# Optimization experiments

Measured on AMD Instinct MI355X. Metric: run time of the kernel, lower is better.

The kernel has to match this reference:

```python
import jax, jax.numpy as jnp
import numpy as np

N, L, S, D, H, DK = 4, 2048, 2048, 1024, 16, 64


def setup_inputs() -> dict:
    key = jax.random.key(0)
    kq, kk, kv, kwq, kwo = jax.random.split(key, 5)
    Q = jax.random.normal(kq, (N, L, D), dtype=jnp.float32)
    K = jax.random.normal(kk, (N, S, D), dtype=jnp.float32)
    V = jax.random.normal(kv, (N, S, D), dtype=jnp.float32)
    # per-head query projection weights (the source reuses Lq for K and V too)
    Wq = jax.random.normal(kwq, (H, DK, D), dtype=jnp.float32) * (D ** -0.5)
    # output projection Lo: Linear(h*dv -> Dv), weight shape (out, in)
    Wo = jax.random.normal(kwo, (D, H * DK), dtype=jnp.float32) * ((H * DK) ** -0.5)
    return {"Q": Q, "K": K, "V": V, "Wq": Wq, "Wo": Wo}


def reference(Q, K, V, Wq, Wo):
    dk = Wq.shape[1]
    # Faithful to source: ALL of q, k, v are projected with the Lq weights.
    q = jnp.einsum('nld,hkd->hnlk', Q, Wq)   # (H,N,L,dk)
    k = jnp.einsum('nsd,hkd->hnsk', K, Wq)   # (H,N,S,dk)
    v = jnp.einsum('nsd,hkd->hnsk', V, Wq)   # (H,N,S,dk)
    scale = jnp.asarray(dk, Q.dtype) ** 0.5
    scores = jnp.einsum('hnlk,hnsk->hnls', q, k) / scale  # (H,N,L,S)
    # Faithful to F.softmax(dot) with no dim on a 3D tensor: torch picks dim=0
    # (the batch axis N); here that is axis=1 of the head-stacked (H,N,L,S).
    attn = jax.nn.softmax(scores, axis=1)
    heads = jnp.einsum('hnls,hnsk->hnlk', attn, v)        # (H,N,L,dk)
    # concat heads along last dim -> (N,L,H*dk)
    heads = jnp.transpose(heads, (1, 2, 0, 3)).reshape(Q.shape[0], Q.shape[1], -1)
    return heads @ Wo.T  # (N,L,Dv)
```

## Files before the change

### kernel.cpp

```cpp
#include <hip/hip_runtime.h>
#include <hip/hip_bf16.h>

typedef __attribute__((ext_vector_type(8))) short short8;
typedef __attribute__((ext_vector_type(4))) short short4v;
typedef __attribute__((ext_vector_type(4))) float float4v;

#define DEVI static __device__ __forceinline__

#if __has_builtin(__builtin_amdgcn_exp2f)
#define EXP2(x) __builtin_amdgcn_exp2f(x)
#else
#define EXP2(x) exp2f(x)
#endif

DEVI unsigned short f2bf(float f) {
  unsigned int u = __builtin_bit_cast(unsigned int, f);
  u += 0x7fffu + ((u >> 16) & 1u);
  return (unsigned short)(u >> 16);
}

DEVI short8 pack8(float4v a, float4v b) {
  struct P4 { __hip_bfloat162 x, y, z, w; } t;
  t.x = __float22bfloat162_rn(make_float2(a[0], a[1]));
  t.y = __float22bfloat162_rn(make_float2(a[2], a[3]));
  t.z = __float22bfloat162_rn(make_float2(b[0], b[1]));
  t.w = __float22bfloat162_rn(make_float2(b[2], b[3]));
  short8 r;
  __builtin_memcpy(&r, &t, 16);
  return r;
}

DEVI short4v pack4(float a, float b, float c, float d) {
  struct P2 { __hip_bfloat162 x, y; } t;
  t.x = __float22bfloat162_rn(make_float2(a, b));
  t.y = __float22bfloat162_rn(make_float2(c, d));
  short4v r;
  __builtin_memcpy(&r, &t, 8);
  return r;
}

DEVI void gload16(const void* src, void* lds_dst) {
  __builtin_amdgcn_global_load_lds(
      (const __attribute__((address_space(1))) void*)src,
      (__attribute__((address_space(3))) void*)lds_dst, 16, 0, 0);
}

template<int AF32, int CMODE>
__global__ __launch_bounds__(256, 2)
void gemm_bt128(const void* __restrict__ Ap, const float* __restrict__ Bp,
                void* __restrict__ Cp, int M, int Nc, int Kd, float oscale)
{
  __shared__ alignas(16) short As[128 * 40];
  __shared__ alignas(16) short Bs[128 * 40];

  const int tid = threadIdx.x;
  const int lane = tid & 63;
  const int wid = tid >> 6;
  const int rl = lane & 15;
  const int g = lane >> 4;
  const int bm = blockIdx.x * 128;
  const int bn = blockIdx.y * 128;
  const int wm = (wid >> 1) * 64;
  const int wn = (wid & 1) * 64;
  const int srow = tid >> 1;
  const int k0 = (tid & 1) * 16;

  float4v acc[4][4];
#pragma unroll
  for (int i = 0; i < 4; ++i)
#pragma unroll
    for (int j = 0; j < 4; ++j) acc[i][j] = (float4v)(0.0f);

  const float* Af = (const float*)Ap;
  const unsigned short* Ab = (const unsigned short*)Ap;

  float4v afr[4], bfr[4];
  short8 ah[2], bh[2];

  const int NK = Kd >> 5;

  auto loadA = [&](int ks) {
    size_t base = (size_t)(bm + srow) * Kd + ks * 32 + k0;
    if constexpr (AF32 != 0) {
      afr[0] = *(const float4v*)(Af + base);
      afr[1] = *(const float4v*)(Af + base + 4);
      afr[2] = *(const float4v*)(Af + base + 8);
      afr[3] = *(const float4v*)(Af + base + 12);
    } else {
      ah[0] = *(const short8*)(Ab + base);
      ah[1] = *(const short8*)(Ab + base + 8);
    }
  };
  auto loadB = [&](int ks) {
    size_t base = (size_t)(bn + srow) * Kd + ks * 32 + k0;
    bfr[0] = *(const float4v*)(Bp + base);
    bfr[1] = *(const float4v*)(Bp + base + 4);
    bfr[2] = *(const float4v*)(Bp + base + 8);
    bfr[3] = *(const float4v*)(Bp + base + 12);
  };

  loadA(0);
  loadB(0);

  for (int ks = 0; ks < NK; ++ks) {
    if constexpr (AF32 != 0) {
      ah[0] = pack8(afr[0], afr[1]);
      ah[1] = pack8(afr[2], afr[3]);
    }
    bh[0] = pack8(bfr[0], bfr[1]);
    bh[1] = pack8(bfr[2], bfr[3]);
    __syncthreads();
    *(short8*)(As + srow * 40 + k0)     = ah[0];
    *(short8*)(As + srow * 40 + k0 + 8) = ah[1];
    *(short8*)(Bs + srow * 40 + k0)     = bh[0];
    *(short8*)(Bs + srow * 40 + k0 + 8) = bh[1];
    __syncthreads();
    if (ks + 1 < NK) { loadA(ks + 1); loadB(ks + 1); }

    short8 a8[4], b8[4];
#pragma unroll
    for (int mt = 0; mt < 4; ++mt)
      a8[mt] = *(const short8*)(As + (wm + mt * 16 + rl) * 40 + 8 * g);
#pragma unroll
    for (int nt = 0; nt < 4; ++nt)
      b8[nt] = *(const short8*)(Bs + (wn + nt * 16 + rl) * 40 + 8 * g);
#pragma unroll
    for (int mt = 0; mt < 4; ++mt)
#pragma unroll
      for (int nt = 0; nt < 4; ++nt)
        acc[mt][nt] = __builtin_amdgcn_mfma_f32_16x16x32_bf16(a8[mt], b8[nt], acc[mt][nt], 0, 0, 0);
  }

#pragma unroll
  for (int mt = 0; mt < 4; ++mt)
#pragma unroll
    for (int nt = 0; nt < 4; ++nt) {
      const int col = bn + wn + nt * 16 + rl;
      const int row0 = bm + wm + mt * 16 + 4 * g;
      if constexpr (CMODE == 1) {
        float* C = (float*)Cp;
#pragma unroll
        for (int r = 0; r < 4; ++r)
          C[(size_t)(row0 + r) * Nc + col] = acc[mt][nt][r];
      } else if constexpr (CMODE == 0) {
        unsigned short* C = (unsigned short*)Cp;
#pragma unroll
        for (int r = 0; r < 4; ++r)
          C[(size_t)(row0 + r) * Nc + col] = f2bf(acc[mt][nt][r] * oscale);
      } else {
        unsigned short* C = (unsigned short*)Cp;
        short4v w = pack4(acc[mt][nt][0], acc[mt][nt][1], acc[mt][nt][2], acc[mt][nt][3]);
        *(short4v*)(C + (size_t)col * M + row0) = w;
      }
    }
}

__global__ __launch_bounds__(512, 2)
void attn_bn(const unsigned short* __restrict__ qb,
             const unsigned short* __restrict__ kb,
             const unsigned short* __restrict__ vtb,
             unsigned short* __restrict__ hb)
{
  __shared__ alignas(128) char smem[131072];

  const int tid = threadIdx.x;
  const int lane = tid & 63;
  const int wid = tid >> 6;
  const int rl = lane & 15;
  const int g = lane >> 4;
  const int h = blockIdx.y;
  const int l0 = blockIdx.x * 128 + wid * 16;

  short8 qf[4][2];
#pragma unroll
  for (int n = 0; n < 4; ++n)
#pragma unroll
    for (int dh = 0; dh < 2; ++dh)
      qf[n][dh] = *(const short8*)(qb + (size_t)(n * 2048 + l0 + rl) * 1024 + h * 64 + dh * 32 + 8 * g);

  float4v ha[4][4];
#pragma unroll
  for (int n = 0; n < 4; ++n)
#pragma unroll
    for (int t = 0; t < 4; ++t) ha[n][t] = (float4v)(0.0f);

  const size_t koff0 = ((size_t)(wid * 2048) + (size_t)(lane >> 3)) * 1024
                     + (size_t)(h * 64) + (size_t)(((lane & 7) ^ (lane >> 3)) * 8);
  const size_t voff0 = ((size_t)(h * 64) + (size_t)(lane >> 2)) * 8192
                     + (size_t)((wid - 4) * 2048)
                     + (size_t)((((lane & 3) ^ ((lane >> 3) & 3)) * 8));

  auto stage = [&](int step, int b) {
    if (wid < 4) {
      char* kdst = smem + b * 32768 + wid * 4096;
      const unsigned short* ksrc = kb + koff0 + (size_t)step * 32 * 1024;
#pragma unroll
      for (int ii = 0; ii < 4; ++ii)
        gload16(ksrc + ii * 8192, kdst + ii * 1024);
    } else {
      char* vdst = smem + b * 32768 + 16384 + (wid - 4) * 4096;
      const unsigned short* vsrc = vtb + voff0 + (size_t)step * 32;
#pragma unroll
      for (int ii = 0; ii < 4; ++ii)
        gload16(vsrc + (size_t)ii * 16 * 8192, vdst + ii * 1024);
    }
  };

  stage(0, 0);
  stage(1, 1);
  stage(2, 2);
  asm volatile("s_waitcnt vmcnt(8)" ::: "memory");
  __builtin_amdgcn_s_barrier();

  const unsigned xr = ((unsigned)((rl >> 1) & 3)) << 4;
  const unsigned half = ((unsigned)(g & 1)) << 3;
  const unsigned voff_lo = (((((unsigned)g >> 1) << 4) ^ xr) + half);
  const unsigned voff_hi = ((((2u + ((unsigned)g >> 1)) << 4) ^ xr) + half);

  for (int to = 0; to < 16; ++to) {
#pragma unroll
    for (int ti = 0; ti < 4; ++ti) {
      const int t = to * 4 + ti;
      char* kbase = smem + ti * 32768;
      char* vbase = kbase + 16384;

      float4v sc[4][2];
#pragma unroll
      for (int n = 0; n < 4; ++n) {
        char* kn = kbase + n * 4096;
#pragma unroll
        for (int ss = 0; ss < 2; ++ss) {
          const int srw = ss * 16 + rl;
          const unsigned sw = ((unsigned)(srw & 7)) << 4;
          short8 kf0 = *(const short8*)(kn + srw * 128 + ((16u * (unsigned)g) ^ sw));
          short8 kf1 = *(const short8*)(kn + srw * 128 + ((64u + 16u * (unsigned)g) ^ sw));
          float4v c = (float4v)(0.0f);
          c = __builtin_amdgcn_mfma_f32_16x16x32_bf16(kf0, qf[n][0], c, 0, 0, 0);
          c = __builtin_amdgcn_mfma_f32_16x16x32_bf16(kf1, qf[n][1], c, 0, 0, 0);
          sc[n][ss] = c;
        }
      }

      short4v pf[2][4];
#pragma unroll
      for (int ss = 0; ss < 2; ++ss) {
        float ex[4][4];
#pragma unroll
        for (int n = 0; n < 4; ++n)
#pragma unroll
          for (int r = 0; r < 4; ++r)
            ex[n][r] = EXP2(fminf(sc[n][ss][r], 24.0f));
#pragma unroll
        for (int r = 0; r < 4; ++r) {
          float inv = __builtin_amdgcn_rcpf((ex[0][r] + ex[1][r]) + (ex[2][r] + ex[3][r]) + 1e-30f);
          ex[0][r] *= inv; ex[1][r] *= inv; ex[2][r] *= inv; ex[3][r] *= inv;
        }
#pragma unroll
        for (int n = 0; n < 4; ++n)
          pf[ss][n] = pack4(ex[n][0], ex[n][1], ex[n][2], ex[n][3]);
      }

#pragma unroll
      for (int n = 0; n < 4; ++n) {
        char* vn = vbase + n * 4096;
        short8 pf8 = __builtin_shufflevector(pf[0][n], pf[1][n], 0, 1, 2, 3, 4, 5, 6, 7);
#pragma unroll
        for (int t4 = 0; t4 < 4; ++t4) {
          const char* rowp = vn + (t4 * 16 + rl) * 64;
          short4v lo = *(const short4v*)(rowp + voff_lo);
          short4v hi = *(const short4v*)(rowp + voff_hi);
          short8 va8 = __builtin_shufflevector(lo, hi, 0, 1, 2, 3, 4, 5, 6, 7);
          ha[n][t4] = __builtin_amdgcn_mfma_f32_16x16x32_bf16(va8, pf8, ha[n][t4], 0, 0, 0);
        }
      }

      if (t + 3 < 64) stage(t + 3, (ti + 3) & 3);
      asm volatile("s_waitcnt vmcnt(8)" ::: "memory");
      __builtin_amdgcn_s_barrier();
    }
  }

#pragma unroll
  for (int n = 0; n < 4; ++n)
#pragma unroll
    for (int tt = 0; tt < 4; ++tt) {
      short4v w = pack4(ha[n][tt][0], ha[n][tt][1], ha[n][tt][2], ha[n][tt][3]);
      size_t off = (size_t)(n * 2048 + l0 + rl) * 1024 + h * 64 + tt * 16 + 4 * g;
      *(short4v*)(hb + off) = w;
    }
}

extern "C" void kernel_launch(void* const* d_in, const int* in_sizes, int n_in,
                              void* d_out, int out_size, void* d_ws, size_t ws_size,
                              hipStream_t stream)
{
  const float* Q  = (const float*)d_in[0];
  const float* K  = (const float*)d_in[1];
  const float* V  = (const float*)d_in[2];
  const float* Wq = (const float*)d_in[3];
  const float* Wo = (const float*)d_in[4];
  float* out = (float*)d_out;

  unsigned short* qb = (unsigned short*)d_ws;
  unsigned short* kw = qb + (size_t)8192 * 1024;
  unsigned short* vt = kw + (size_t)8192 * 1024;
  unsigned short* hw = qb;

  const float CS = 0.18033688011112042f;

  dim3 gg(64, 8), bb(256);
  gemm_bt128<1, 0><<<gg, bb, 0, stream>>>(Q, Wq, qb, 8192, 1024, 1024, CS);
  gemm_bt128<1, 0><<<gg, bb, 0, stream>>>(K, Wq, kw, 8192, 1024, 1024, 1.0f);
  gemm_bt128<1, 2><<<gg, bb, 0, stream>>>(V, Wq, vt, 8192, 1024, 1024, 1.0f);
  attn_bn<<<dim3(16, 16), dim3(512), 0, stream>>>(qb, kw, vt, hw);
  gemm_bt128<0, 1><<<gg, bb, 0, stream>>>(hw, Wo, out, 8192, 1024, 1024, 1.0f);
}
```

Baseline: 274.8 us.

## Split attention over key range with atomic fp32 accumulation and smaller LDS

Splits the attention kernel's key dimension in two across a new grid z axis, doubling block count. It halves the shared-memory ring to two stages so more blocks fit per CU, and replaces the bf16 head write with fp32 atomic adds into a zeroed output buffer. The output GEMM then reads fp32 heads and writes to workspace, followed by a device copy back to the output. This adds a memset, atomics, a larger fp32 intermediate read and an extra copy, and the prefetch depth drops from three stages to one.

Result: slower. 949.9 us (+245.7%).

```diff
diff --git a/kernel.cpp b/kernel.cpp
--- a/kernel.cpp
+++ b/kernel.cpp
@@ -155,13 +155,13 @@
     }
 }
 
-__global__ __launch_bounds__(512, 2)
+__global__ __launch_bounds__(512, 4)
 void attn_bn(const unsigned short* __restrict__ qb,
              const unsigned short* __restrict__ kb,
              const unsigned short* __restrict__ vtb,
-             unsigned short* __restrict__ hb)
+             float* __restrict__ outf)
 {
-  __shared__ alignas(128) char smem[131072];
+  __shared__ alignas(128) char smem[65536];
 
   const int tid = threadIdx.x;
   const int lane = tid & 63;
@@ -169,6 +169,7 @@
   const int rl = lane & 15;
   const int g = lane >> 4;
   const int h = blockIdx.y;
+  const int z = blockIdx.z;
   const int l0 = blockIdx.x * 128 + wid * 16;
 
   short8 qf[4][2];
@@ -184,10 +185,10 @@
 #pragma unroll
     for (int t = 0; t < 4; ++t) ha[n][t] = (float4v)(0.0f);
 
-  const size_t koff0 = ((size_t)(wid * 2048) + (size_t)(lane >> 3)) * 1024
+  const size_t koff0 = ((size_t)(wid * 2048 + z * 1024) + (size_t)(lane >> 3)) * 1024
                      + (size_t)(h * 64) + (size_t)(((lane & 7) ^ (lane >> 3)) * 8);
   const size_t voff0 = ((size_t)(h * 64) + (size_t)(lane >> 2)) * 8192
-                     + (size_t)((wid - 4) * 2048)
+                     + (size_t)((wid - 4) * 2048 + z * 1024)
                      + (size_t)((((lane & 3) ^ ((lane >> 3) & 3)) * 8));
 
   auto stage = [&](int step, int b) {
@@ -207,22 +208,19 @@
   };
 
   stage(0, 0);
-  stage(1, 1);
-  stage(2, 2);
-  asm volatile("s_waitcnt vmcnt(8)" ::: "memory");
-  __builtin_amdgcn_s_barrier();
+  __syncthreads();
 
   const unsigned xr = ((unsigned)((rl >> 1) & 3)) << 4;
   const unsigned half = ((unsigned)(g & 1)) << 3;
-  const unsigned voff_lo = (((((unsigned)g >> 1) << 4) ^ xr) + half);
-  const unsigned voff_hi = ((((2u + ((unsigned)g >> 1)) << 4) ^ xr) + half);
 
   for (int to = 0; to < 16; ++to) {
 #pragma unroll
-    for (int ti = 0; ti < 4; ++ti) {
-      const int t = to * 4 + ti;
+    for (int ti = 0; ti < 2; ++ti) {
+      const int t = to * 2 + ti;
       char* kbase = smem + ti * 32768;
       char* vbase = kbase + 16384;
+
+      if (t + 1 < 32) stage(t + 1, ti ^ 1);
 
       float4v sc[4][2];
 #pragma unroll
@@ -241,7 +239,6 @@
         }
       }
 
-      short4v pf[2][4];
 #pragma unroll
       for (int ss = 0; ss < 2; ++ss) {
         float ex[4][4];
@@ -255,28 +252,29 @@
           float inv = __builtin_amdgcn_rcpf((ex[0][r] + ex[1][r]) + (ex[2][r] + ex[3][r]) + 1e-30f);
           ex[0][r] *= inv; ex[1][r] *= inv; ex[2][r] *= inv; ex[3][r] *= inv;
         }
-#pragma unroll
-        for (int n = 0; n < 4; ++n)
-          pf[ss][n] = pack4(ex[n][0], ex[n][1], ex[n][2], ex[n][3]);
-      }
-
-#pragma unroll
-      for (int n = 0; n < 4; ++n) {
-        char* vn = vbase + n * 4096;
-        short8 pf8 = __builtin_shufflevector(pf[0][n], pf[1][n], 0, 1, 2, 3, 4, 5, 6, 7);
-#pragma unroll
-        for (int t4 = 0; t4 < 4; ++t4) {
-          const char* rowp = vn + (t4 * 16 + rl) * 64;
-          short4v lo = *(const short4v*)(rowp + voff_lo);
-          short4v hi = *(const short4v*)(rowp + voff_hi);
-          short8 va8 = __builtin_shufflevector(lo, hi, 0, 1, 2, 3, 4, 5, 6, 7);
-          ha[n][t4] = __builtin_amdgcn_mfma_f32_16x16x32_bf16(va8, pf8, ha[n][t4], 0, 0, 0);
+        short4v pf[4];
+#pragma unroll
+        for (int n = 0; n < 4; ++n) {
+          unsigned lo = (unsigned)f2bf(ex[n][0]) | ((unsigned)f2bf(ex[n][1]) << 16);
+          unsigned hi = (unsigned)f2bf(ex[n][2]) | ((unsigned)f2bf(ex[n][3]) << 16);
+          uint2 u; u.x = lo; u.y = hi;
+          pf[n] = __builtin_bit_cast(short4v, u);
+        }
+
+        const unsigned chunk0 = 2u * (unsigned)ss + ((unsigned)g >> 1);
+#pragma unroll
+        for (int n = 0; n < 4; ++n) {
+          char* vn = vbase + n * 4096;
+#pragma unroll
+          for (int t4 = 0; t4 < 4; ++t4) {
+            const char* rowp = vn + (t4 * 16 + rl) * 64;
+            short4v va = *(const short4v*)(rowp + (((chunk0 << 4) ^ xr) + half));
+            ha[n][t4] = __builtin_amdgcn_mfma_f32_16x16x16bf16_1k(va, pf[n], ha[n][t4], 0, 0, 0);
+          }
         }
       }
 
-      if (t + 3 < 64) stage(t + 3, (ti + 3) & 3);
-      asm volatile("s_waitcnt vmcnt(8)" ::: "memory");
-      __builtin_amdgcn_s_barrier();
+      __syncthreads();
     }
   }
 
@@ -284,9 +282,10 @@
   for (int n = 0; n < 4; ++n)
 #pragma unroll
     for (int tt = 0; tt < 4; ++tt) {
-      short4v w = pack4(ha[n][tt][0], ha[n][tt][1], ha[n][tt][2], ha[n][tt][3]);
       size_t off = (size_t)(n * 2048 + l0 + rl) * 1024 + h * 64 + tt * 16 + 4 * g;
-      *(short4v*)(hb + off) = w;
+#pragma unroll
+      for (int r = 0; r < 4; ++r)
+        unsafeAtomicAdd(outf + off + r, ha[n][tt][r]);
     }
 }
 
@@ -304,14 +303,17 @@
   unsigned short* qb = (unsigned short*)d_ws;
   unsigned short* kw = qb + (size_t)8192 * 1024;
   unsigned short* vt = kw + (size_t)8192 * 1024;
-  unsigned short* hw = qb;
+  float* cbuf = (float*)d_ws;
 
   const float CS = 0.18033688011112042f;
 
   dim3 gg(64, 8), bb(256);
+  hipMemsetAsync(d_out, 0, (size_t)out_size * sizeof(float), stream);
   gemm_bt128<1, 0><<<gg, bb, 0, stream>>>(Q, Wq, qb, 8192, 1024, 1024, CS);
   gemm_bt128<1, 0><<<gg, bb, 0, stream>>>(K, Wq, kw, 8192, 1024, 1024, 1.0f);
   gemm_bt128<1, 2><<<gg, bb, 0, stream>>>(V, Wq, vt, 8192, 1024, 1024, 1.0f);
-  attn_bn<<<dim3(16, 16), dim3(512), 0, stream>>>(qb, kw, vt, hw);
-  gemm_bt128<0, 1><<<gg, bb, 0, stream>>>(hw, Wo, out, 8192, 1024, 1024, 1.0f);
-}
+  attn_bn<<<dim3(16, 16, 2), dim3(512), 0, stream>>>(qb, kw, vt, (float*)d_out);
+  gemm_bt128<1, 1><<<gg, bb, 0, stream>>>(d_out, Wo, cbuf, 8192, 1024, 1024, 1.0f);
+  hipMemcpyAsync(d_out, cbuf, (size_t)out_size * sizeof(float),
+                 hipMemcpyDeviceToDevice, stream);
+}
```

## Double-buffer GEMM LDS tiles and split PV MFMA into per-half 16x16x16 ops

Applied to the files above, without the earlier changes.

The projection GEMM now keeps two LDS buffers and writes the next tile after the current MFMAs. This drops one barrier per k-step and lets the LDS stores overlap compute. In attention, the PV product is issued per score half as 16x16x16 MFMAs as soon as each half's probabilities are packed, instead of building an 8-wide operand from both halves. That shortens register live ranges and removes the shuffles, but doubles the MFMA instruction count and doubles LDS use in the GEMM, which may hurt occupancy.

Result: no change. 273.5 us (-0.5%).

```diff
diff --git a/kernel.cpp b/kernel.cpp
--- a/kernel.cpp
+++ b/kernel.cpp
@@ -50,8 +50,8 @@
 void gemm_bt128(const void* __restrict__ Ap, const float* __restrict__ Bp,
                 void* __restrict__ Cp, int M, int Nc, int Kd, float oscale)
 {
-  __shared__ alignas(16) short As[128 * 40];
-  __shared__ alignas(16) short Bs[128 * 40];
+  __shared__ alignas(16) short As[2][128 * 40];
+  __shared__ alignas(16) short Bs[2][128 * 40];
 
   const int tid = threadIdx.x;
   const int lane = tid & 63;
@@ -98,37 +98,49 @@
     bfr[2] = *(const float4v*)(Bp + base + 8);
     bfr[3] = *(const float4v*)(Bp + base + 12);
   };
-
-  loadA(0);
-  loadB(0);
-
-  for (int ks = 0; ks < NK; ++ks) {
+  auto packAB = [&]() {
     if constexpr (AF32 != 0) {
       ah[0] = pack8(afr[0], afr[1]);
       ah[1] = pack8(afr[2], afr[3]);
     }
     bh[0] = pack8(bfr[0], bfr[1]);
     bh[1] = pack8(bfr[2], bfr[3]);
-    __syncthreads();
-    *(short8*)(As + srow * 40 + k0)     = ah[0];
-    *(short8*)(As + srow * 40 + k0 + 8) = ah[1];
-    *(short8*)(Bs + srow * 40 + k0)     = bh[0];
-    *(short8*)(Bs + srow * 40 + k0 + 8) = bh[1];
-    __syncthreads();
+  };
+  auto writeLDS = [&](int b) {
+    *(short8*)(As[b] + srow * 40 + k0)     = ah[0];
+    *(short8*)(As[b] + srow * 40 + k0 + 8) = ah[1];
+    *(short8*)(Bs[b] + srow * 40 + k0)     = bh[0];
+    *(short8*)(Bs[b] + srow * 40 + k0 + 8) = bh[1];
+  };
+
+  loadA(0);
+  loadB(0);
+  packAB();
+  writeLDS(0);
+  __syncthreads();
+
+  for (int ks = 0; ks < NK; ++ks) {
     if (ks + 1 < NK) { loadA(ks + 1); loadB(ks + 1); }
 
+    const int b = ks & 1;
     short8 a8[4], b8[4];
 #pragma unroll
     for (int mt = 0; mt < 4; ++mt)
-      a8[mt] = *(const short8*)(As + (wm + mt * 16 + rl) * 40 + 8 * g);
+      a8[mt] = *(const short8*)(As[b] + (wm + mt * 16 + rl) * 40 + 8 * g);
 #pragma unroll
     for (int nt = 0; nt < 4; ++nt)
-      b8[nt] = *(const short8*)(Bs + (wn + nt * 16 + rl) * 40 + 8 * g);
+      b8[nt] = *(const short8*)(Bs[b] + (wn + nt * 16 + rl) * 40 + 8 * g);
 #pragma unroll
     for (int mt = 0; mt < 4; ++mt)
 #pragma unroll
       for (int nt = 0; nt < 4; ++nt)
         acc[mt][nt] = __builtin_amdgcn_mfma_f32_16x16x32_bf16(a8[mt], b8[nt], acc[mt][nt], 0, 0, 0);
+
+    if (ks + 1 < NK) {
+      packAB();
+      writeLDS(b ^ 1);
+    }
+    __syncthreads();
   }
 
 #pragma unroll
@@ -214,8 +226,6 @@
 
   const unsigned xr = ((unsigned)((rl >> 1) & 3)) << 4;
   const unsigned half = ((unsigned)(g & 1)) << 3;
-  const unsigned voff_lo = (((((unsigned)g >> 1) << 4) ^ xr) + half);
-  const unsigned voff_hi = ((((2u + ((unsigned)g >> 1)) << 4) ^ xr) + half);
 
   for (int to = 0; to < 16; ++to) {
 #pragma unroll
@@ -241,7 +251,6 @@
         }
       }
 
-      short4v pf[2][4];
 #pragma unroll
       for (int ss = 0; ss < 2; ++ss) {
         float ex[4][4];
@@ -255,22 +264,21 @@
           float inv = __builtin_amdgcn_rcpf((ex[0][r] + ex[1][r]) + (ex[2][r] + ex[3][r]) + 1e-30f);
           ex[0][r] *= inv; ex[1][r] *= inv; ex[2][r] *= inv; ex[3][r] *= inv;
         }
+        short4v pf[4];
 #pragma unroll
         for (int n = 0; n < 4; ++n)
-          pf[ss][n] = pack4(ex[n][0], ex[n][1], ex[n][2], ex[n][3]);
-      }
-
-#pragma unroll
-      for (int n = 0; n < 4; ++n) {
-        char* vn = vbase + n * 4096;
-        short8 pf8 = __builtin_shufflevector(pf[0][n], pf[1][n], 0, 1, 2, 3, 4, 5, 6, 7);
-#pragma unroll
-        for (int t4 = 0; t4 < 4; ++t4) {
-          const char* rowp = vn + (t4 * 16 + rl) * 64;
-          short4v lo = *(const short4v*)(rowp + voff_lo);
-          short4v hi = *(const short4v*)(rowp + voff_hi);
-          short8 va8 = __builtin_shufflevector(lo, hi, 0, 1, 2, 3, 4, 5, 6, 7);
-          ha[n][t4] = __builtin_amdgcn_mfma_f32_16x16x32_bf16(va8, pf8, ha[n][t4], 0, 0, 0);
+          pf[n] = pack4(ex[n][0], ex[n][1], ex[n][2], ex[n][3]);
+
+        const unsigned chunk0 = 2u * (unsigned)ss + ((unsigned)g >> 1);
+#pragma unroll
+        for (int n = 0; n < 4; ++n) {
+          char* vn = vbase + n * 4096;
+#pragma unroll
+          for (int t4 = 0; t4 < 4; ++t4) {
+            const char* rowp = vn + (t4 * 16 + rl) * 64;
+            short4v va = *(const short4v*)(rowp + (((chunk0 << 4) ^ xr) + half));
+            ha[n][t4] = __builtin_amdgcn_mfma_f32_16x16x16bf16_1k(va, pf[n], ha[n][t4], 0, 0, 0);
+          }
         }
       }
 
@@ -299,7 +307,6 @@
   const float* V  = (const float*)d_in[2];
   const float* Wq = (const float*)d_in[3];
   const float* Wo = (const float*)d_in[4];
-  float* out = (float*)d_out;
 
   unsigned short* qb = (unsigned short*)d_ws;
   unsigned short* kw = qb + (size_t)8192 * 1024;
@@ -313,5 +320,5 @@
   gemm_bt128<1, 0><<<gg, bb, 0, stream>>>(K, Wq, kw, 8192, 1024, 1024, 1.0f);
   gemm_bt128<1, 2><<<gg, bb, 0, stream>>>(V, Wq, vt, 8192, 1024, 1024, 1.0f);
   attn_bn<<<dim3(16, 16), dim3(512), 0, stream>>>(qb, kw, vt, hw);
-  gemm_bt128<0, 1><<<gg, bb, 0, stream>>>(hw, Wo, out, 8192, 1024, 1024, 1.0f);
-}
+  gemm_bt128<0, 1><<<gg, bb, 0, stream>>>(hw, Wo, (float*)d_out, 8192, 1024, 1024, 1.0f);
+}
```
